# Optimization experiments

Measured on AMD Instinct MI355X. Metric: run time of the kernel, lower is better.

## Reference

```python
import jax, jax.numpy as jnp
import numpy as np

N = 100000   # nodes
E = 1600000  # edges (before self-loops)
IN, HID, OUT = 256, 128, 64
NEG_SLOPE = 0.2  # PyG GATConv default


def setup_inputs() -> dict:
    key = jax.random.key(0)
    ks = jax.random.split(key, 12)
    s = 0.05
    return {
        "x": jax.random.normal(ks[0], (N, IN), jnp.float32),
        "edge_index": jax.random.randint(ks[1], (2, E), 0, N, dtype=jnp.int32),
        "W1": jax.random.normal(ks[2], (IN, HID), jnp.float32) * s,
        "a1_src": jax.random.normal(ks[3], (HID,), jnp.float32) * s,
        "a1_dst": jax.random.normal(ks[4], (HID,), jnp.float32) * s,
        "b1": jnp.zeros((HID,), jnp.float32),
        "W2": jax.random.normal(ks[5], (HID, OUT), jnp.float32) * s,
        "a2_src": jax.random.normal(ks[6], (OUT,), jnp.float32) * s,
        "a2_dst": jax.random.normal(ks[7], (OUT,), jnp.float32) * s,
        "b2": jnp.zeros((OUT,), jnp.float32),
    }


def _gat_conv(x, src, dst, W, a_src, a_dst, b):
    """Single-head PyG GATConv (concat=True, heads=1), self-loops already in src/dst."""
    h = x @ W                                   # [N, F]
    alpha_s = h @ a_src                         # [N]
    alpha_d = h @ a_dst                         # [N]
    e = jax.nn.leaky_relu(alpha_s[src] + alpha_d[dst], NEG_SLOPE)  # [E+N]
    # segment softmax over edges grouped by destination node
    m = jax.ops.segment_max(e, dst, num_segments=N)                # [N]
    ex = jnp.exp(e - m[dst])
    denom = jax.ops.segment_sum(ex, dst, num_segments=N)           # [N]
    coef = ex / denom[dst]                                         # [E+N]
    out = jax.ops.segment_sum(h[src] * coef[:, None], dst, num_segments=N)
    return out + b


def reference(x, edge_index, W1, a1_src, a1_dst, b1, W2, a2_src, a2_dst, b2):
    loops = jnp.arange(N, dtype=edge_index.dtype)
    src = jnp.concatenate([edge_index[0], loops])
    dst = jnp.concatenate([edge_index[1], loops])
    h = _gat_conv(x, src, dst, W1, a1_src, a1_dst, b1)
    h = jax.nn.relu(h)
    # dropout is identity at inference (training=False)
    out = _gat_conv(h, src, dst, W2, a2_src, a2_dst, b2)
    return out
```

## Files before the change

### kernel.cpp

```cpp
#include <hip/hip_runtime.h>
#include <hip/hip_bf16.h>
#include <cstdint>

#define N_NODES 100000
#define N_EDGES 1600000
#define F_IN 256
#define F_HID 128
#define F_OUT 64
#define NEG_SLOPE 0.2f

#define BSH 7
#define NB 782
#define CAP 3072
#define CAPS 3072
#define NBLK_E 256

typedef __attribute__((ext_vector_type(8))) short bf16x8;
typedef __attribute__((ext_vector_type(4))) float f32x4;

__device__ __forceinline__ ushort f2bf(float f) {
  uint u = __float_as_uint(f);
  u += 0x7fffu + ((u >> 16) & 1u);
  return (ushort)(u >> 16);
}
__device__ __forceinline__ float bf2f(ushort s) {
  return __uint_as_float(((uint)s) << 16);
}
__device__ __forceinline__ uint pack2(float a, float b) {
  return (uint)f2bf(a) | ((uint)f2bf(b) << 16);
}

__global__ void wprep_kernel(const float* __restrict__ W, ushort* __restrict__ Wt,
                             int K, int Ncol) {
  int i = blockIdx.x * blockDim.x + threadIdx.x;
  if (i < K * Ncol) {
    int k = i / Ncol, c = i % Ncol;
    Wt[(size_t)c * K + k] = f2bf(W[i]);
  }
}

template <int BN, int K, bool AF32>
__global__ __launch_bounds__(256) void gemm_mfma(
    const void* __restrict__ Ap, const ushort* __restrict__ Bt,
    ushort* __restrict__ Cb, const float* __restrict__ a_src,
    const float* __restrict__ a_dst, float* __restrict__ as_,
    float* __restrict__ ad_, int M) {
  constexpr int CT = BN / 16;
  __shared__ __align__(16) ushort Alds[128 * 32];
  __shared__ __align__(16) ushort Blds[BN * 32];
  const int tid = threadIdx.x;
  const int wave = tid >> 6, lane = tid & 63;
  const int lr = lane & 15, lq = lane >> 4;
  const int gm0 = blockIdx.x * 128;

  f32x4 acc[2][CT];
#pragma unroll
  for (int a = 0; a < 2; ++a)
#pragma unroll
    for (int b = 0; b < CT; ++b)
#pragma unroll
      for (int e = 0; e < 4; ++e) acc[a][b][e] = 0.f;

  for (int kt = 0; kt < K; kt += 32) {
#pragma unroll
    for (int i = 0; i < 2; ++i) {
      int sid = i * 256 + tid;
      int row = sid >> 2, q = sid & 3;
      int gm = gm0 + row;
      uint4 w = make_uint4(0u, 0u, 0u, 0u);
      if (gm < M) {
        if (AF32) {
          const float* s = (const float*)Ap + (size_t)gm * K + kt + q * 8;
          float4 u = *(const float4*)s;
          float4 v = *(const float4*)(s + 4);
          w.x = pack2(u.x, u.y); w.y = pack2(u.z, u.w);
          w.z = pack2(v.x, v.y); w.w = pack2(v.z, v.w);
        } else {
          w = *(const uint4*)((const ushort*)Ap + (size_t)gm * K + kt + q * 8);
        }
      }
      int phys = row * 4 + (q ^ ((row >> 2) & 3));
      *(uint4*)&Alds[phys * 8] = w;
    }
#pragma unroll
    for (int i = 0; i < BN * 4 / 256; ++i) {
      int sid = i * 256 + tid;
      int row = sid >> 2, q = sid & 3;
      uint4 w = *(const uint4*)(Bt + (size_t)row * K + kt + q * 8);
      int phys = row * 4 + (q ^ ((row >> 2) & 3));
      *(uint4*)&Blds[phys * 8] = w;
    }
    __syncthreads();

    bf16x8 af[2], bfr[CT];
#pragma unroll
    for (int rt = 0; rt < 2; ++rt) {
      int r = wave * 32 + rt * 16 + lr;
      af[rt] = *(const bf16x8*)&Alds[(r * 4 + (lq ^ ((r >> 2) & 3))) * 8];
    }
#pragma unroll
    for (int c = 0; c < CT; ++c) {
      int r = c * 16 + lr;
      bfr[c] = *(const bf16x8*)&Blds[(r * 4 + (lq ^ ((r >> 2) & 3))) * 8];
    }
#pragma unroll
    for (int rt = 0; rt < 2; ++rt)
#pragma unroll
      for (int c = 0; c < CT; ++c)
        acc[rt][c] = __builtin_amdgcn_mfma_f32_16x16x32_bf16(af[rt], bfr[c], acc[rt][c], 0, 0, 0);
    __syncthreads();
  }

#pragma unroll
  for (int rt = 0; rt < 2; ++rt)
#pragma unroll
    for (int ri = 0; ri < 4; ++ri) {
      int gr = gm0 + wave * 32 + rt * 16 + lq * 4 + ri;
      if (gr < M) {
#pragma unroll
        for (int c = 0; c < CT; ++c)
          Cb[(size_t)gr * BN + c * 16 + lr] = f2bf(acc[rt][c][ri]);
      }
    }

  float avs[CT], avd[CT];
#pragma unroll
  for (int c = 0; c < CT; ++c) {
    avs[c] = a_src[c * 16 + lr];
    avd[c] = a_dst[c * 16 + lr];
  }
#pragma unroll
  for (int rt = 0; rt < 2; ++rt)
#pragma unroll
    for (int ri = 0; ri < 4; ++ri) {
      int gr = gm0 + wave * 32 + rt * 16 + lq * 4 + ri;
      float s = 0.f, d = 0.f;
#pragma unroll
      for (int c = 0; c < CT; ++c) {
        float hv = acc[rt][c][ri];
        s += hv * avs[c];
        d += hv * avd[c];
      }
#pragma unroll
      for (int off = 1; off < 16; off <<= 1) {
        s += __shfl_xor(s, off);
        d += __shfl_xor(d, off);
      }
      if (gr < M && lr == 0) {
        as_[gr] = s;
        ad_[gr] = d;
      }
    }
}


__global__ __launch_bounds__(256) void ehist_kernel(const int* __restrict__ dst,
                                                    int* __restrict__ hist_blk) {
  __shared__ int h[NB];
  for (int t = threadIdx.x; t < NB; t += 256) h[t] = 0;
  __syncthreads();
  const int per = (N_EDGES + NBLK_E - 1) / NBLK_E;
  const int e0 = blockIdx.x * per;
  const int e1 = min(e0 + per, N_EDGES);
  for (int i = e0 + threadIdx.x; i < e1; i += 256)
    atomicAdd(&h[dst[i] >> BSH], 1);
  __syncthreads();
  for (int t = threadIdx.x; t < NB; t += 256)
    hist_blk[blockIdx.x * NB + t] = h[t];
}

__global__ __launch_bounds__(NBLK_E) void escan_kernel(int* __restrict__ hist_blk,
                                                       int* __restrict__ btotal) {
  __shared__ int sh[NBLK_E];
  const int j = blockIdx.x, t = threadIdx.x;
  int v = hist_blk[t * NB + j];
  sh[t] = v;
  __syncthreads();
  for (int off = 1; off < NBLK_E; off <<= 1) {
    int x = (t >= off) ? sh[t - off] : 0;
    __syncthreads();
    sh[t] += x;
    __syncthreads();
  }
  hist_blk[t * NB + j] = sh[t] - v;
  if (t == NBLK_E - 1) btotal[j] = sh[NBLK_E - 1];
}

__global__ __launch_bounds__(256) void escatter_kernel(
    const int* __restrict__ src, const int* __restrict__ dst,
    const int* __restrict__ hist_blk, uint* __restrict__ staged) {
  __shared__ int cur[NB];
  for (int t = threadIdx.x; t < NB; t += 256)
    cur[t] = hist_blk[blockIdx.x * NB + t];
  __syncthreads();
  const int per = (N_EDGES + NBLK_E - 1) / NBLK_E;
  const int e0 = blockIdx.x * per;
  const int e1 = min(e0 + per, N_EDGES);
  for (int i = e0 + threadIdx.x; i < e1; i += 256) {
    int d = dst[i];
    int b = d >> BSH;
    int p = atomicAdd(&cur[b], 1);
    if (p < CAPS)
      staged[(size_t)b * CAPS + p] = ((uint)src[i] << BSH) | (uint)(d & ((1 << BSH) - 1));
  }
}

__global__ __launch_bounds__(256) void fine_kernel(
    const uint* __restrict__ staged, const int* __restrict__ btotal,
    int* __restrict__ counts, int* __restrict__ offs, int* __restrict__ csr_src) {
  __shared__ int hist[128];
  __shared__ int cur[128];
  const int b = blockIdx.x, t = threadIdx.x;
  const int n0 = b << BSH;
  const int nn = min(128, N_NODES - n0);
  if (t < 128) hist[t] = 0;
  __syncthreads();
  const int ce = min(btotal[b], CAPS);
  const uint* sp = staged + (size_t)b * CAPS;
  for (int i = t; i < ce; i += 256)
    atomicAdd(&hist[sp[i] & 127], 1);
  __syncthreads();
  int v = 0;
  if (t < 128) {
    v = (t < nn) ? hist[t] + 1 : 0;
    cur[t] = v;
  }
  __syncthreads();
  for (int off = 1; off < 128; off <<= 1) {
    int x = 0;
    if (t < 128 && t >= off) x = cur[t - off];
    __syncthreads();
    if (t < 128) cur[t] += x;
    __syncthreads();
  }
  int excl = (t < 128) ? cur[t] - v : 0;
  __syncthreads();
  if (t < nn) {
    counts[n0 + t] = v;
    offs[n0 + t] = b * CAP + excl;
    csr_src[b * CAP + excl] = n0 + t;
    cur[t] = excl + 1;
  }
  __syncthreads();
  for (int i = t; i < ce; i += 256) {
    uint e = sp[i];
    int p = atomicAdd(&cur[e & 127], 1);
    csr_src[b * CAP + p] = (int)(e >> BSH);
  }
}

template <int C, bool RELU, bool OUTBF>
__global__ __launch_bounds__(256) void agg_kernel(
    const ushort* __restrict__ h, const float* __restrict__ as_,
    const float* __restrict__ ad_, const int* __restrict__ offs,
    const int* __restrict__ counts, const int* __restrict__ csr_src,
    const float* __restrict__ bias, void* __restrict__ outp, int M) {
  int wid = (int)((blockIdx.x * (size_t)blockDim.x + threadIdx.x) >> 6);
  int lane = threadIdx.x & 63;
  if (wid >= M) return;
  const int start = offs[wid];
  const int cnt = counts[wid];
  const float adn = ad_[wid];

  float m = -3.402823e38f, ssum = 0.f;
  for (int j = lane; j < cnt; j += 64) {
    float e = as_[csr_src[start + j]] + adn;
    e = (e >= 0.f) ? e : NEG_SLOPE * e;
    float mn = fmaxf(m, e);
    ssum = ssum * __expf(m - mn) + __expf(e - mn);
    m = mn;
  }
#pragma unroll
  for (int off = 32; off; off >>= 1) {
    float mo = __shfl_xor(m, off), so = __shfl_xor(ssum, off);
    float mn = fmaxf(m, mo);
    ssum = ssum * __expf(m - mn) + so * __expf(mo - mn);
    m = mn;
  }
  const float inv = 1.0f / ssum;

  float acc0 = 0.f, acc1 = 0.f;
  for (int j0 = 0; j0 < cnt; j0 += 64) {
    int j = j0 + lane;
    int sj = 0;
    float pj = 0.f;
    if (j < cnt) {
      sj = csr_src[start + j];
      float e = as_[sj] + adn;
      e = (e >= 0.f) ? e : NEG_SLOPE * e;
      pj = __expf(e - m) * inv;
    }
    int c2 = min(64, cnt - j0);
    int jj = 0;
    for (; jj + 8 <= c2; jj += 8) {
      float pp[8];
      if (C == 128) {
        uint vv[8];
#pragma unroll
        for (int q = 0; q < 8; ++q) {
          int sq = __shfl(sj, jj + q);
          pp[q] = __shfl(pj, jj + q);
          vv[q] = ((const uint*)(h + (size_t)sq * C))[lane];
        }
#pragma unroll
        for (int q = 0; q < 8; ++q) {
          acc0 += pp[q] * bf2f((ushort)(vv[q] & 0xffffu));
          acc1 += pp[q] * bf2f((ushort)(vv[q] >> 16));
        }
      } else {
        ushort vv[8];
#pragma unroll
        for (int q = 0; q < 8; ++q) {
          int sq = __shfl(sj, jj + q);
          pp[q] = __shfl(pj, jj + q);
          vv[q] = h[(size_t)sq * C + lane];
        }
#pragma unroll
        for (int q = 0; q < 8; ++q) acc0 += pp[q] * bf2f(vv[q]);
      }
    }
    for (; jj < c2; ++jj) {
      int s0 = __shfl(sj, jj);
      float p0 = __shfl(pj, jj);
      if (C == 128) {
        uint v0 = ((const uint*)(h + (size_t)s0 * C))[lane];
        acc0 += p0 * bf2f((ushort)(v0 & 0xffffu));
        acc1 += p0 * bf2f((ushort)(v0 >> 16));
      } else {
        acc0 += p0 * bf2f(h[(size_t)s0 * C + lane]);
      }
    }
  }

  if (C == 128) {
    float r0 = acc0 + bias[2 * lane];
    float r1 = acc1 + bias[2 * lane + 1];
    if (RELU) {
      r0 = fmaxf(r0, 0.f);
      r1 = fmaxf(r1, 0.f);
    }
    if (OUTBF)
      ((uint*)outp)[(size_t)wid * (C / 2) + lane] = pack2(r0, r1);
    else
      ((float2*)outp)[(size_t)wid * (C / 2) + lane] = make_float2(r0, r1);
  } else {
    float r0 = acc0 + bias[lane];
    if (RELU) r0 = fmaxf(r0, 0.f);
    if (OUTBF)
      ((ushort*)outp)[(size_t)wid * C + lane] = f2bf(r0);
    else
      ((float*)outp)[(size_t)wid * C + lane] = r0;
  }
}

extern "C" void kernel_launch(void* const* d_in, const int* in_sizes, int n_in,
                              void* d_out, int out_size, void* d_ws, size_t ws_size,
                              hipStream_t stream) {
  const float* x = (const float*)d_in[0];
  const int* ei = (const int*)d_in[1];
  const float* W1 = (const float*)d_in[2];
  const float* a1s = (const float*)d_in[3];
  const float* a1d = (const float*)d_in[4];
  const float* b1 = (const float*)d_in[5];
  const float* W2 = (const float*)d_in[6];
  const float* a2s = (const float*)d_in[7];
  const float* a2d = (const float*)d_in[8];
  const float* b2 = (const float*)d_in[9];
  float* out = (float*)d_out;

  const int* esrc = ei;
  const int* edst = ei + N_EDGES;

  char* ws = (char*)d_ws;
  size_t off = 0;
  auto alloc = [&](size_t bytes) {
    size_t o = off;
    off = (off + bytes + 255) & ~(size_t)255;
    return o;
  };
  ushort* h1b = (ushort*)(ws + alloc((size_t)N_NODES * F_HID * 2));
  ushort* hrb = (ushort*)(ws + alloc((size_t)N_NODES * F_HID * 2));
  ushort* h2b = (ushort*)(ws + alloc((size_t)N_NODES * F_OUT * 2));
  float* as1 = (float*)(ws + alloc((size_t)N_NODES * 4));
  float* ad1 = (float*)(ws + alloc((size_t)N_NODES * 4));
  float* as2 = (float*)(ws + alloc((size_t)N_NODES * 4));
  float* ad2 = (float*)(ws + alloc((size_t)N_NODES * 4));
  int* counts = (int*)(ws + alloc((size_t)N_NODES * 4));
  int* offs = (int*)(ws + alloc((size_t)N_NODES * 4));
  int* hist_blk = (int*)(ws + alloc((size_t)NBLK_E * NB * 4));
  int* btotal = (int*)(ws + alloc((size_t)NB * 4));
  uint* staged = (uint*)(ws + alloc((size_t)NB * CAPS * 4));
  int* csr_src = (int*)(ws + alloc((size_t)NB * CAP * 4));
  ushort* W1t = (ushort*)(ws + alloc((size_t)F_IN * F_HID * 2));
  ushort* W2t = (ushort*)(ws + alloc((size_t)F_HID * F_OUT * 2));

  ehist_kernel<<<NBLK_E, 256, 0, stream>>>(edst, hist_blk);
  escan_kernel<<<NB, NBLK_E, 0, stream>>>(hist_blk, btotal);
  escatter_kernel<<<NBLK_E, 256, 0, stream>>>(esrc, edst, hist_blk, staged);
  fine_kernel<<<NB, 256, 0, stream>>>(staged, btotal, counts, offs, csr_src);

  wprep_kernel<<<(F_IN * F_HID + 255) / 256, 256, 0, stream>>>(W1, W1t, F_IN, F_HID);
  wprep_kernel<<<(F_HID * F_OUT + 255) / 256, 256, 0, stream>>>(W2, W2t, F_HID, F_OUT);

  gemm_mfma<F_HID, F_IN, true><<<(N_NODES + 127) / 128, 256, 0, stream>>>(
      x, W1t, h1b, a1s, a1d, as1, ad1, N_NODES);
  agg_kernel<F_HID, true, true><<<(N_NODES + 3) / 4, 256, 0, stream>>>(
      h1b, as1, ad1, offs, counts, csr_src, b1, hrb, N_NODES);

  gemm_mfma<F_OUT, F_HID, false><<<(N_NODES + 127) / 128, 256, 0, stream>>>(
      hrb, W2t, h2b, a2s, a2d, as2, ad2, N_NODES);
  agg_kernel<F_OUT, false, false><<<(N_NODES + 3) / 4, 256, 0, stream>>>(
      h2b, as2, ad2, offs, counts, csr_src, b2, out, N_NODES);
}
```

Before: 421.8 us.

## Rework GAT aggregation: half-wave edge split for C=64, readlane broadcast, cached first chunk

In the aggregation kernel, the first 64 source indices and logits from the softmax pass are now kept in registers and reused, so the first chunk does not reload csr_src and as_. For C=128, neighbor broadcast uses readlane instead of shfl and the gather is unrolled 16 deep. For C=64, each half-wave handles a different edge and loads packed bf16 pairs as 32-bit words, then the halves are summed with a cross-half shuffle. This should widen memory transactions and raise loads in flight, at the cost of more registers and extra tail-handling logic.

New measurement: 401.6 us. 4.8% less time.

```diff
diff --git a/kernel.cpp b/kernel.cpp
--- a/kernel.cpp
+++ b/kernel.cpp
@@ -153,7 +153,6 @@
     }
 }
 
-
 __global__ __launch_bounds__(256) void ehist_kernel(const int* __restrict__ dst,
                                                     int* __restrict__ hist_blk) {
   __shared__ int h[NB];
@@ -263,9 +262,13 @@
   const float adn = ad_[wid];
 
   float m = -3.402823e38f, ssum = 0.f;
+  int sj0 = 0;
+  float e0 = -3.402823e38f;
   for (int j = lane; j < cnt; j += 64) {
-    float e = as_[csr_src[start + j]] + adn;
+    int sj = csr_src[start + j];
+    float e = as_[sj] + adn;
     e = (e >= 0.f) ? e : NEG_SLOPE * e;
+    if (j < 64) { sj0 = sj; e0 = e; }
     float mn = fmaxf(m, e);
     ssum = ssum * __expf(m - mn) + __expf(e - mn);
     m = mn;
@@ -279,62 +282,101 @@
   }
   const float inv = 1.0f / ssum;
 
-  float acc0 = 0.f, acc1 = 0.f;
+  float2 acc = make_float2(0.f, 0.f);
+  const int half = lane >> 5;
+  const int cl = lane & 31;
+
   for (int j0 = 0; j0 < cnt; j0 += 64) {
     int j = j0 + lane;
-    int sj = 0;
-    float pj = 0.f;
-    if (j < cnt) {
-      sj = csr_src[start + j];
-      float e = as_[sj] + adn;
-      e = (e >= 0.f) ? e : NEG_SLOPE * e;
-      pj = __expf(e - m) * inv;
+    int sj;
+    float pj;
+    if (j0 == 0) {
+      sj = sj0;
+      pj = __expf(e0 - m) * inv;
+    } else {
+      sj = 0;
+      pj = 0.f;
+      if (j < cnt) {
+        sj = csr_src[start + j];
+        float e = as_[sj] + adn;
+        e = (e >= 0.f) ? e : NEG_SLOPE * e;
+        pj = __expf(e - m) * inv;
+      }
     }
     int c2 = min(64, cnt - j0);
     int jj = 0;
-    for (; jj + 8 <= c2; jj += 8) {
-      float pp[8];
-      if (C == 128) {
+    if (C == 128) {
+      for (; jj + 16 <= c2; jj += 16) {
+        uint vv[16];
+        float pp[16];
+#pragma unroll
+        for (int q = 0; q < 16; ++q) {
+          int sq = __builtin_amdgcn_readlane(sj, jj + q);
+          pp[q] = __uint_as_float((uint)__builtin_amdgcn_readlane((int)__float_as_uint(pj), jj + q));
+          vv[q] = *((const uint*)(h + (size_t)sq * C) + lane);
+        }
+#pragma unroll
+        for (int q = 0; q < 16; ++q) {
+          acc.x = fmaf(pp[q], bf2f((ushort)(vv[q] & 0xffffu)), acc.x);
+          acc.y = fmaf(pp[q], bf2f((ushort)(vv[q] >> 16)), acc.y);
+        }
+      }
+      for (; jj + 4 <= c2; jj += 4) {
+        uint vv[4];
+        float pp[4];
+#pragma unroll
+        for (int q = 0; q < 4; ++q) {
+          int sq = __builtin_amdgcn_readlane(sj, jj + q);
+          pp[q] = __uint_as_float((uint)__builtin_amdgcn_readlane((int)__float_as_uint(pj), jj + q));
+          vv[q] = *((const uint*)(h + (size_t)sq * C) + lane);
+        }
+#pragma unroll
+        for (int q = 0; q < 4; ++q) {
+          acc.x = fmaf(pp[q], bf2f((ushort)(vv[q] & 0xffffu)), acc.x);
+          acc.y = fmaf(pp[q], bf2f((ushort)(vv[q] >> 16)), acc.y);
+        }
+      }
+      for (; jj < c2; ++jj) {
+        int sq = __builtin_amdgcn_readlane(sj, jj);
+        float pq = __uint_as_float((uint)__builtin_amdgcn_readlane((int)__float_as_uint(pj), jj));
+        uint v = *((const uint*)(h + (size_t)sq * C) + lane);
+        acc.x = fmaf(pq, bf2f((ushort)(v & 0xffffu)), acc.x);
+        acc.y = fmaf(pq, bf2f((ushort)(v >> 16)), acc.y);
+      }
+    } else {
+      const uint* h32 = (const uint*)h;
+      for (; jj + 16 <= c2; jj += 16) {
         uint vv[8];
+        float pp[8];
 #pragma unroll
         for (int q = 0; q < 8; ++q) {
-          int sq = __shfl(sj, jj + q);
-          pp[q] = __shfl(pj, jj + q);
-          vv[q] = ((const uint*)(h + (size_t)sq * C))[lane];
+          int idx = jj + 2 * q + half;
+          int sq = __shfl(sj, idx);
+          pp[q] = __shfl(pj, idx);
+          vv[q] = h32[(size_t)sq * (C / 2) + cl];
         }
 #pragma unroll
         for (int q = 0; q < 8; ++q) {
-          acc0 += pp[q] * bf2f((ushort)(vv[q] & 0xffffu));
-          acc1 += pp[q] * bf2f((ushort)(vv[q] >> 16));
-        }
-      } else {
-        ushort vv[8];
-#pragma unroll
-        for (int q = 0; q < 8; ++q) {
-          int sq = __shfl(sj, jj + q);
-          pp[q] = __shfl(pj, jj + q);
-          vv[q] = h[(size_t)sq * C + lane];
-        }
-#pragma unroll
-        for (int q = 0; q < 8; ++q) acc0 += pp[q] * bf2f(vv[q]);
-      }
-    }
-    for (; jj < c2; ++jj) {
-      int s0 = __shfl(sj, jj);
-      float p0 = __shfl(pj, jj);
-      if (C == 128) {
-        uint v0 = ((const uint*)(h + (size_t)s0 * C))[lane];
-        acc0 += p0 * bf2f((ushort)(v0 & 0xffffu));
-        acc1 += p0 * bf2f((ushort)(v0 >> 16));
-      } else {
-        acc0 += p0 * bf2f(h[(size_t)s0 * C + lane]);
+          acc.x = fmaf(pp[q], bf2f((ushort)(vv[q] & 0xffffu)), acc.x);
+          acc.y = fmaf(pp[q], bf2f((ushort)(vv[q] >> 16)), acc.y);
+        }
+      }
+      for (; jj < c2; jj += 2) {
+        int idx = jj + half;
+        int idc = min(idx, c2 - 1);
+        int sq = __shfl(sj, idc);
+        float pq = __shfl(pj, idc);
+        if (idx >= c2) pq = 0.f;
+        uint v = h32[(size_t)sq * (C / 2) + cl];
+        acc.x = fmaf(pq, bf2f((ushort)(v & 0xffffu)), acc.x);
+        acc.y = fmaf(pq, bf2f((ushort)(v >> 16)), acc.y);
       }
     }
   }
 
   if (C == 128) {
-    float r0 = acc0 + bias[2 * lane];
-    float r1 = acc1 + bias[2 * lane + 1];
+    float r0 = acc.x + bias[2 * lane];
+    float r1 = acc.y + bias[2 * lane + 1];
     if (RELU) {
       r0 = fmaxf(r0, 0.f);
       r1 = fmaxf(r1, 0.f);
@@ -344,12 +386,20 @@
     else
       ((float2*)outp)[(size_t)wid * (C / 2) + lane] = make_float2(r0, r1);
   } else {
-    float r0 = acc0 + bias[lane];
-    if (RELU) r0 = fmaxf(r0, 0.f);
-    if (OUTBF)
-      ((ushort*)outp)[(size_t)wid * C + lane] = f2bf(r0);
-    else
-      ((float*)outp)[(size_t)wid * C + lane] = r0;
+    acc.x += __shfl_xor(acc.x, 32);
+    acc.y += __shfl_xor(acc.y, 32);
+    if (lane < 32) {
+      float r0 = acc.x + bias[2 * cl];
+      float r1 = acc.y + bias[2 * cl + 1];
+      if (RELU) {
+        r0 = fmaxf(r0, 0.f);
+        r1 = fmaxf(r1, 0.f);
+      }
+      if (OUTBF)
+        ((uint*)outp)[(size_t)wid * (C / 2) + cl] = pack2(r0, r1);
+      else
+        ((float2*)outp)[(size_t)wid * (C / 2) + cl] = make_float2(r0, r1);
+    }
   }
 }
 
```
